# Kernel tuning notes

Measured on AMD Instinct MI355X. Metric: run time of the kernel, lower is better.

## Reference

```python
import jax, jax.numpy as jnp
import numpy as np

N = 400000        # pixel nodes (B images ~224x224)
E = 3200000       # edges, avg degree 8
B = 8             # images
NUM_SP = 150      # superpixels per image (<= 196, per assert)
S = B * NUM_SP    # total superpixel segments
GRID = 14 * 14    # fixed 14x14 grid = 196 slots
DIMS = [24, 8, 16, 32, 64, 64]  # conv_out_dim=24 -> channels//8 ... channels=64


def setup_inputs():
    key = jax.random.key(0)
    ks = jax.random.split(key, 16)
    inp = {}
    inp["x"] = jax.random.normal(ks[0], (N, DIMS[0]), jnp.float32)
    inp["edge_index"] = jax.random.randint(ks[1], (2, E), 0, N, jnp.int32)
    inp["batch_idx"] = jnp.sort(jax.random.randint(ks[2], (N,), 0, S, jnp.int32))
    inp["num_sp"] = jnp.full((B,), NUM_SP, jnp.int32)
    for i in range(5):
        fi, fo = DIMS[i], DIMS[i + 1]
        inp[f"W{i+1}"] = jax.random.normal(ks[3 + i], (fi, fo), jnp.float32) * (2.0 / fi) ** 0.5
        inp[f"b{i+1}"] = jnp.zeros((fo,), jnp.float32)
        inp[f"g{i+1}"] = jnp.ones((fo,), jnp.float32)
        inp[f"be{i+1}"] = jnp.zeros((fo,), jnp.float32)
    C = DIMS[-1]
    inp["Wp"] = jax.random.normal(ks[9], (4 * C, C), jnp.float32) * (2.0 / (4 * C)) ** 0.5
    inp["bp"] = jnp.zeros((C,), jnp.float32)
    return inp


def _forward(x, edge_index, batch_idx, num_sp, layers, Wp, bp):
    n = x.shape[0]
    # GCNConv: add self-loops, symmetric normalization D^-1/2 (A+I) D^-1/2
    loop = jnp.arange(n, dtype=edge_index.dtype)
    src = jnp.concatenate([edge_index[0], loop])
    dst = jnp.concatenate([edge_index[1], loop])
    deg = jax.ops.segment_sum(jnp.ones_like(dst, dtype=jnp.float32), dst, num_segments=n)
    dis = jax.lax.rsqrt(deg)  # deg >= 1 due to self-loops
    norm = dis[src] * dis[dst]  # [E+N]

    h = x
    for i, (W, b, g, be) in enumerate(layers):
        h = h @ W                                                   # [N, fo]
        h = jax.ops.segment_sum(h[src] * norm[:, None], dst, num_segments=n) + b
        # BatchNorm (training mode: batch stats over all nodes)
        mu = h.mean(axis=0)
        var = h.var(axis=0)
        h = g * (h - mu) * jax.lax.rsqrt(var + 1e-5) + be
        if i < 4:  # last BN feeds the aggregator directly (no ReLU)
            h = jax.nn.relu(h)

    # MultiAggregation(['mean','min','max','std'], mode='proj') over superpixel ids
    cnt = jnp.maximum(jax.ops.segment_sum(jnp.ones((n, 1), jnp.float32), batch_idx, num_segments=S), 1.0)
    sm = jax.ops.segment_sum(h, batch_idx, num_segments=S)
    sm2 = jax.ops.segment_sum(h * h, batch_idx, num_segments=S)
    mean = sm / cnt
    std = jnp.sqrt(jax.nn.relu(sm2 / cnt - mean * mean) + 1e-5)  # PyG StdAggregation
    mn = jax.ops.segment_min(h, batch_idx, num_segments=S)
    mx = jax.ops.segment_max(h, batch_idx, num_segments=S)
    agg = jnp.concatenate([mean, mn, mx, std], axis=1) @ Wp + bp  # [S, C]

    # padding_reshape_layer: pack per-image superpixel rows into [B, C, 14, 14]
    offs = jnp.cumsum(num_sp) - num_sp                # start row of each image
    pos = jnp.arange(GRID, dtype=num_sp.dtype)
    idx = jnp.clip(offs[:, None] + pos[None, :], 0, S - 1)  # [B, 196]
    mask = pos[None, :] < num_sp[:, None]
    feats = jnp.where(mask[..., None], agg[idx], 0.0)       # [B, 196, C]
    C = agg.shape[1]
    # torch: reshape(14,14,C) then transpose(0,2) -> y[c,j,i] = x[i,j,c]
    return feats.reshape(B, 14, 14, C).transpose(0, 3, 2, 1)


def reference(x, edge_index, batch_idx, num_sp,
              W1, b1, g1, be1, W2, b2, g2, be2, W3, b3, g3, be3,
              W4, b4, g4, be4, W5, b5, g5, be5, Wp, bp):
    layers = [(W1, b1, g1, be1), (W2, b2, g2, be2), (W3, b3, g3, be3),
              (W4, b4, g4, be4), (W5, b5, g5, be5)]
    return _forward(x, edge_index, batch_idx, num_sp, layers, Wp, bp)
```

## Files before the change

kernel.cpp:

```cpp
#include <hip/hip_runtime.h>
#include <hip/hip_fp16.h>

#define TPB 256
#define BSH 9
#define BUCK (1 << BSH)
#define NBMAX 1024
#define CAP 6144

using f16x8 = __attribute__((ext_vector_type(8))) _Float16;
using f32x4 = __attribute__((ext_vector_type(4))) float;


union H8 { uint4 u; __half2 h[4]; f16x8 f; };
union H4 { uint2 u; __half2 h[2]; };

__device__ inline void h8_to_f(const H8 v, float4& a, float4& b) {
    float2 f0 = __half22float2(v.h[0]);
    float2 f1 = __half22float2(v.h[1]);
    float2 f2 = __half22float2(v.h[2]);
    float2 f3 = __half22float2(v.h[3]);
    a = make_float4(f0.x, f0.y, f1.x, f1.y);
    b = make_float4(f2.x, f2.y, f3.x, f3.y);
}
__device__ inline H8 f_to_h8(float4 a, float4 b) {
    H8 r;
    r.h[0] = __floats2half2_rn(a.x, a.y);
    r.h[1] = __floats2half2_rn(a.z, a.w);
    r.h[2] = __floats2half2_rn(b.x, b.y);
    r.h[3] = __floats2half2_rn(b.z, b.w);
    return r;
}
__device__ inline float4 f4z() { return make_float4(0.f, 0.f, 0.f, 0.f); }
__device__ inline float4 f4axpy(float4 a, float s, float4 c) {
    return make_float4(fmaf(a.x, s, c.x), fmaf(a.y, s, c.y), fmaf(a.z, s, c.z), fmaf(a.w, s, c.w));
}
__device__ inline float4 f4relu_aff(float4 h, float4 sc, float4 sb) {
    return make_float4(fmaxf(fmaf(h.x, sc.x, sb.x), 0.f), fmaxf(fmaf(h.y, sc.y, sb.y), 0.f),
                       fmaxf(fmaf(h.z, sc.z, sb.z), 0.f), fmaxf(fmaf(h.w, sc.w, sb.w), 0.f));
}


__global__ __launch_bounds__(256) void k_bcount(const int* __restrict__ dst, int E,
                                                int* __restrict__ bcount, int nb) {
    __shared__ int hist[NBMAX];
    for (int i = threadIdx.x; i < nb; i += 256) hist[i] = 0;
    __syncthreads();
    const int e0 = blockIdx.x * 8192;
#pragma unroll 4
    for (int k = 0; k < 32; ++k) {
        int e = e0 + k * 256 + threadIdx.x;
        if (e < E) atomicAdd(&hist[dst[e] >> BSH], 1);
    }
    __syncthreads();
    for (int i = threadIdx.x; i < nb; i += 256) {
        int h = hist[i];
        if (h) atomicAdd(&bcount[i], h);
    }
}

__global__ void k_bscan(const int* __restrict__ bcount, int* __restrict__ bbase,
                        int* __restrict__ bcur, int nb, int E, int* __restrict__ row_ptr,
                        int n) {
    if (threadIdx.x == 0 && blockIdx.x == 0) {
        int run = 0;
        for (int i = 0; i < nb; ++i) {
            bbase[i] = run;
            bcur[i] = run;
            run += bcount[i];
        }
        bbase[nb] = E;
        row_ptr[n] = E;
    }
}

__global__ __launch_bounds__(256) void k_partA(const int* __restrict__ src,
                                               const int* __restrict__ dst, int E,
                                               int* __restrict__ bcur, int* __restrict__ bin,
                                               int nb) {
    __shared__ int hist[NBMAX];
    __shared__ int base[NBMAX];
    for (int i = threadIdx.x; i < nb; i += 256) hist[i] = 0;
    __syncthreads();
    const int e0 = blockIdx.x * 8192;
#pragma unroll 4
    for (int k = 0; k < 32; ++k) {
        int e = e0 + k * 256 + threadIdx.x;
        if (e < E) atomicAdd(&hist[dst[e] >> BSH], 1);
    }
    __syncthreads();
    for (int i = threadIdx.x; i < nb; i += 256) {
        int h = hist[i];
        base[i] = h ? atomicAdd(&bcur[i], h) : 0;
        hist[i] = 0;
    }
    __syncthreads();
#pragma unroll 4
    for (int k = 0; k < 32; ++k) {
        int e = e0 + k * 256 + threadIdx.x;
        if (e < E) {
            int d = dst[e];
            int b = d >> BSH;
            int off = atomicAdd(&hist[b], 1);
            bin[base[b] + off] = ((d & (BUCK - 1)) << 19) | src[e];
        }
    }
}

__global__ __launch_bounds__(256) void k_csr_bucket(const int* __restrict__ bin,
                                                    const int* __restrict__ bbase,
                                                    int* __restrict__ row_ptr,
                                                    float* __restrict__ dis,
                                                    int* __restrict__ csr_src, int n) {
    __shared__ int ldeg[BUCK];
    __shared__ int lcur[BUCK];
    __shared__ int ts[256];
    __shared__ int stage[CAP];
    const int b = blockIdx.x;
    const int node0 = b << BSH;
    const int nodes = min(BUCK, n - node0);
    const int ebeg = bbase[b], eend = bbase[b + 1];
    const int cnt = eend - ebeg;

    for (int i = threadIdx.x; i < BUCK; i += 256) ldeg[i] = 0;
    __syncthreads();
    for (int e = ebeg + threadIdx.x; e < eend; e += 256)
        atomicAdd(&ldeg[bin[e] >> 19], 1);
    __syncthreads();

    const int b2 = threadIdx.x * 2;
    int v0 = ldeg[b2], v1 = ldeg[b2 + 1];
    ts[threadIdx.x] = v0 + v1;
    __syncthreads();
    for (int off = 1; off < 256; off <<= 1) {
        int t = (threadIdx.x >= off) ? ts[threadIdx.x - off] : 0;
        __syncthreads();
        ts[threadIdx.x] += t;
        __syncthreads();
    }
    int o0 = (threadIdx.x == 0) ? 0 : ts[threadIdx.x - 1];
    int o1 = o0 + v0;
    lcur[b2] = o0;
    lcur[b2 + 1] = o1;
    if (b2 < nodes) {
        row_ptr[node0 + b2] = ebeg + o0;
        dis[node0 + b2] = rsqrtf((float)(v0 + 1));
    }
    if (b2 + 1 < nodes) {
        row_ptr[node0 + b2 + 1] = ebeg + o1;
        dis[node0 + b2 + 1] = rsqrtf((float)(v1 + 1));
    }
    __syncthreads();

    for (int e = ebeg + threadIdx.x; e < eend; e += 256) {
        int p = bin[e];
        int pos = atomicAdd(&lcur[p >> 19], 1);
        int s = p & 0x7FFFF;
        if (pos < CAP) stage[pos] = s;
        else csr_src[ebeg + pos] = s;
    }
    __syncthreads();
    int m = cnt < CAP ? cnt : CAP;
    for (int i = threadIdx.x; i < m; i += 256) csr_src[ebeg + i] = stage[i];
}


template <int FI, int FO, bool STATS, bool IN_F32>
__global__ __launch_bounds__(TPB) void k_mm_v(const void* __restrict__ tin,
                                              const float* __restrict__ W,
                                              __half* __restrict__ z,
                                              float* __restrict__ stats, int n) {
    constexpr int GROUPS = FO / 8;
    constexpr int NPB = (TPB / GROUPS) * 4;
    __shared__ float sW[FI * FO];
    __shared__ float sred[STATS ? TPB * 16 : 1];
    for (int i = threadIdx.x; i < FI * FO; i += TPB) sW[i] = W[i];
    __syncthreads();

    const int g = threadIdx.x % GROUPS;
    const int nl = threadIdx.x / GROUPS;
    const int nbase = blockIdx.x * NPB + nl * 4;

    float4 acc0[4], acc1[4];
#pragma unroll
    for (int j = 0; j < 4; ++j) { acc0[j] = f4z(); acc1[j] = f4z(); }

    for (int k = 0; k < FI; k += 4) {
        float4 wv0[4], wv1[4];
#pragma unroll
        for (int kk = 0; kk < 4; ++kk) {
            wv0[kk] = *(const float4*)&sW[(k + kk) * FO + g * 8];
            wv1[kk] = *(const float4*)&sW[(k + kk) * FO + g * 8 + 4];
        }
#pragma unroll
        for (int j = 0; j < 4; ++j) {
            int node = nbase + j;
            float rk[4] = {0.f, 0.f, 0.f, 0.f};
            if (node < n) {
                if (IN_F32) {
                    float4 rv = *(const float4*)((const float*)tin + (size_t)node * FI + k);
                    rk[0] = rv.x; rk[1] = rv.y; rk[2] = rv.z; rk[3] = rv.w;
                } else {
                    H4 hv;
                    hv.u = *(const uint2*)((const __half*)tin + (size_t)node * FI + k);
                    float2 f0 = __half22float2(hv.h[0]);
                    float2 f1 = __half22float2(hv.h[1]);
                    rk[0] = f0.x; rk[1] = f0.y; rk[2] = f1.x; rk[3] = f1.y;
                }
            }
#pragma unroll
            for (int kk = 0; kk < 4; ++kk) {
                acc0[j] = f4axpy(wv0[kk], rk[kk], acc0[j]);
                acc1[j] = f4axpy(wv1[kk], rk[kk], acc1[j]);
            }
        }
    }

#pragma unroll
    for (int j = 0; j < 4; ++j) {
        int node = nbase + j;
        if (node < n) {
            H8 o = f_to_h8(acc0[j], acc1[j]);
            *(uint4*)(z + (size_t)node * FO + g * 8) = o.u;
        }
    }

    if (STATS) {
        float4 s0 = f4z(), s1 = f4z(), q0 = f4z(), q1 = f4z();
#pragma unroll
        for (int j = 0; j < 4; ++j) {
            s0.x += acc0[j].x; s0.y += acc0[j].y; s0.z += acc0[j].z; s0.w += acc0[j].w;
            s1.x += acc1[j].x; s1.y += acc1[j].y; s1.z += acc1[j].z; s1.w += acc1[j].w;
            q0.x = fmaf(acc0[j].x, acc0[j].x, q0.x); q0.y = fmaf(acc0[j].y, acc0[j].y, q0.y);
            q0.z = fmaf(acc0[j].z, acc0[j].z, q0.z); q0.w = fmaf(acc0[j].w, acc0[j].w, q0.w);
            q1.x = fmaf(acc1[j].x, acc1[j].x, q1.x); q1.y = fmaf(acc1[j].y, acc1[j].y, q1.y);
            q1.z = fmaf(acc1[j].z, acc1[j].z, q1.z); q1.w = fmaf(acc1[j].w, acc1[j].w, q1.w);
        }
        float* slot = &sred[threadIdx.x * 16];
        *(float4*)(slot + 0) = s0;
        *(float4*)(slot + 4) = s1;
        *(float4*)(slot + 8) = q0;
        *(float4*)(slot + 12) = q1;
        __syncthreads();
        if (threadIdx.x < FO * 2) {
            int c = threadIdx.x % FO;
            int m = threadIdx.x / FO;
            int g2 = c / 8, ci = c % 8;
            float a = 0.f;
            for (int nl2 = 0; nl2 < TPB / GROUPS; ++nl2)
                a += sred[(nl2 * GROUPS + g2) * 16 + m * 8 + ci];
            atomicAdd(&stats[m * FO + c], a);
        }
    }
}


template <int FI, int RT>
__global__ __launch_bounds__(256) void k_gmm(const int* __restrict__ row_ptr,
                                             const int* __restrict__ csr_src,
                                             const float* __restrict__ dis,
                                             const __half* __restrict__ zin,
                                             const float* __restrict__ W,
                                             const float* __restrict__ stats_in,
                                             const float* __restrict__ gg,
                                             const float* __restrict__ be, float inv_n,
                                             __half* __restrict__ zout,
                                             float* __restrict__ stats_out, int n) {
    constexpr int KC = FI / 32;
    constexpr int RSW = FI + 8;
    constexpr int ROWS = 4 * RT * 16;
    __shared__ _Float16 wt[64 * RSW];
    __shared__ float saff[2 * FI];
    __shared__ float sstat[2][4][64];

    for (int i = threadIdx.x; i < FI * 64; i += 256) {
        int k = i >> 6, nn = i & 63;
        wt[nn * RSW + k] = (_Float16)W[i];
    }
    if (threadIdx.x < FI) {
        int c = threadIdx.x;
        float mu = stats_in[c] * inv_n;
        float var = stats_in[FI + c] * inv_n - mu * mu;
        float sv = gg[c] * rsqrtf(var + 1e-5f);
        saff[c] = sv;
        saff[FI + c] = fmaf(-mu, sv, be[c]);
    }
    __syncthreads();

    const int lane = threadIdx.x & 63;
    const int wv = threadIdx.x >> 6;
    const int quad = lane >> 4;
    const int mcol = lane & 15;

    f16x8 bf[4][KC];
#pragma unroll
    for (int t = 0; t < 4; ++t)
#pragma unroll
        for (int c = 0; c < KC; ++c)
            bf[t][c] = *(const f16x8*)&wt[(t * 16 + mcol) * RSW + c * 32 + quad * 8];

    float4 sc[2 * KC], sb[2 * KC];
#pragma unroll
    for (int c = 0; c < KC; ++c) {
        sc[2 * c] = *(const float4*)&saff[c * 32 + quad * 8];
        sc[2 * c + 1] = *(const float4*)&saff[c * 32 + quad * 8 + 4];
        sb[2 * c] = *(const float4*)&saff[FI + c * 32 + quad * 8];
        sb[2 * c + 1] = *(const float4*)&saff[FI + c * 32 + quad * 8 + 4];
    }

    float s[4] = {0.f, 0.f, 0.f, 0.f}, q[4] = {0.f, 0.f, 0.f, 0.f};

#pragma unroll
    for (int rt = 0; rt < RT; ++rt) {
        const int row0 = blockIdx.x * ROWS + wv * (RT * 16) + rt * 16;
        const int node = row0 + mcol;
        float4 acc[2 * KC];
#pragma unroll
        for (int v = 0; v < 2 * KC; ++v) acc[v] = f4z();

        if (node < n) {
            float dn = dis[node];
            float w0 = dn * dn;
#pragma unroll
            for (int c = 0; c < KC; ++c) {
                H8 hv;
                hv.u = *(const uint4*)(zin + (size_t)node * FI + c * 32 + quad * 8);
                float4 a, b;
                h8_to_f(hv, a, b);
                a = f4relu_aff(a, sc[2 * c], sb[2 * c]);
                b = f4relu_aff(b, sc[2 * c + 1], sb[2 * c + 1]);
                acc[2 * c] = f4axpy(a, w0, acc[2 * c]);
                acc[2 * c + 1] = f4axpy(b, w0, acc[2 * c + 1]);
            }
            int beg = row_ptr[node], end = row_ptr[node + 1];
            int j = beg;
            for (; j + 1 < end; j += 2) {
                int s0 = csr_src[j], s1 = csr_src[j + 1];
                float wA = dn * dis[s0];
                float wB = dn * dis[s1];
                uint4 rA[KC], rB[KC];
#pragma unroll
                for (int c = 0; c < KC; ++c) {
                    rA[c] = *(const uint4*)(zin + (size_t)s0 * FI + c * 32 + quad * 8);
                    rB[c] = *(const uint4*)(zin + (size_t)s1 * FI + c * 32 + quad * 8);
                }
#pragma unroll
                for (int c = 0; c < KC; ++c) {
                    H8 hv; float4 a, b;
                    hv.u = rA[c];
                    h8_to_f(hv, a, b);
                    a = f4relu_aff(a, sc[2 * c], sb[2 * c]);
                    b = f4relu_aff(b, sc[2 * c + 1], sb[2 * c + 1]);
                    acc[2 * c] = f4axpy(a, wA, acc[2 * c]);
                    acc[2 * c + 1] = f4axpy(b, wA, acc[2 * c + 1]);
                    hv.u = rB[c];
                    h8_to_f(hv, a, b);
                    a = f4relu_aff(a, sc[2 * c], sb[2 * c]);
                    b = f4relu_aff(b, sc[2 * c + 1], sb[2 * c + 1]);
                    acc[2 * c] = f4axpy(a, wB, acc[2 * c]);
                    acc[2 * c + 1] = f4axpy(b, wB, acc[2 * c + 1]);
                }
            }
            if (j < end) {
                int s0 = csr_src[j];
                float wA = dn * dis[s0];
#pragma unroll
                for (int c = 0; c < KC; ++c) {
                    H8 hv;
                    hv.u = *(const uint4*)(zin + (size_t)s0 * FI + c * 32 + quad * 8);
                    float4 a, b;
                    h8_to_f(hv, a, b);
                    a = f4relu_aff(a, sc[2 * c], sb[2 * c]);
                    b = f4relu_aff(b, sc[2 * c + 1], sb[2 * c + 1]);
                    acc[2 * c] = f4axpy(a, wA, acc[2 * c]);
                    acc[2 * c + 1] = f4axpy(b, wA, acc[2 * c + 1]);
                }
            }
        }

        f16x8 a[KC];
#pragma unroll
        for (int c = 0; c < KC; ++c) {
            H8 cv = f_to_h8(acc[2 * c], acc[2 * c + 1]);
            a[c] = cv.f;
        }
        f32x4 cacc[4];
#pragma unroll
        for (int t = 0; t < 4; ++t) cacc[t] = f32x4{0.f, 0.f, 0.f, 0.f};
#pragma unroll
        for (int t = 0; t < 4; ++t)
#pragma unroll
            for (int c = 0; c < KC; ++c)
                cacc[t] = __builtin_amdgcn_mfma_f32_16x16x32_f16(a[c], bf[t][c], cacc[t], 0, 0, 0);

#pragma unroll
        for (int t = 0; t < 4; ++t)
#pragma unroll
            for (int r = 0; r < 4; ++r) {
                int row = row0 + quad * 4 + r;
                if (row < n) zout[(size_t)row * 64 + t * 16 + mcol] = __float2half(cacc[t][r]);
            }
#pragma unroll
        for (int t = 0; t < 4; ++t) {
            s[t] += cacc[t][0] + cacc[t][1] + cacc[t][2] + cacc[t][3];
            q[t] += cacc[t][0] * cacc[t][0] + cacc[t][1] * cacc[t][1] + cacc[t][2] * cacc[t][2] +
                    cacc[t][3] * cacc[t][3];
        }
    }

#pragma unroll
    for (int off = 16; off < 64; off <<= 1) {
#pragma unroll
        for (int t = 0; t < 4; ++t) {
            s[t] += __shfl_xor(s[t], off, 64);
            q[t] += __shfl_xor(q[t], off, 64);
        }
    }
    if (lane < 16) {
#pragma unroll
        for (int t = 0; t < 4; ++t) {
            sstat[0][wv][t * 16 + lane] = s[t];
            sstat[1][wv][t * 16 + lane] = q[t];
        }
    }
    __syncthreads();
    if (threadIdx.x < 128) {
        int c = threadIdx.x & 63, m = threadIdx.x >> 6;
        float a4 = sstat[m][0][c] + sstat[m][1][c] + sstat[m][2][c] + sstat[m][3][c];
        atomicAdd(&stats_out[m * 64 + c], a4);
    }
}


template <int F, bool AFFINE, bool STATS>
__global__ __launch_bounds__(TPB) void k_gather(const int* __restrict__ row_ptr,
                                                const int* __restrict__ csr_src,
                                                const float* __restrict__ dis,
                                                const __half* __restrict__ z,
                                                __half* __restrict__ t,
                                                const float* __restrict__ stats_in,
                                                const float* __restrict__ gg,
                                                const float* __restrict__ be, float inv_n,
                                                float* __restrict__ stats_out, int n) {
    constexpr int GW = (F < 16) ? F : 16;
    constexpr int PARTS = F / GW;
    constexpr int NV = GW / 4;
    constexpr int NL = GW / 8;
    __shared__ float sred[STATS ? TPB * 16 : 1];
    int tid = blockIdx.x * blockDim.x + threadIdx.x;
    int node = tid / PARTS;
    int part = tid % PARTS;
    bool active = node < n;
    if (!STATS && !active) return;
    const int cbase = part * GW;

    float4 sc[NV], sb[NV];
    if (AFFINE) {
#pragma unroll
        for (int v = 0; v < NV; ++v) {
            float scv[4], sbv[4];
#pragma unroll
            for (int u = 0; u < 4; ++u) {
                int c = cbase + v * 4 + u;
                float mu = stats_in[c] * inv_n;
                float var = stats_in[F + c] * inv_n - mu * mu;
                float s = gg[c] * rsqrtf(var + 1e-5f);
                scv[u] = s;
                sbv[u] = fmaf(-mu, s, be[c]);
            }
            sc[v] = make_float4(scv[0], scv[1], scv[2], scv[3]);
            sb[v] = make_float4(sbv[0], sbv[1], sbv[2], sbv[3]);
        }
    }

    float4 acc[NV];
#pragma unroll
    for (int v = 0; v < NV; ++v) acc[v] = f4z();

    if (active) {
        float dn = dis[node];
        float w0 = dn * dn;
        {
            const uint4* zp = (const uint4*)(z + (size_t)node * F + cbase);
#pragma unroll
            for (int l = 0; l < NL; ++l) {
                H8 hv; hv.u = zp[l];
                float4 a, b;
                h8_to_f(hv, a, b);
                if (AFFINE) { a = f4relu_aff(a, sc[2 * l], sb[2 * l]); b = f4relu_aff(b, sc[2 * l + 1], sb[2 * l + 1]); }
                acc[2 * l] = f4axpy(a, w0, acc[2 * l]);
                acc[2 * l + 1] = f4axpy(b, w0, acc[2 * l + 1]);
            }
        }
        int beg = row_ptr[node], end = row_ptr[node + 1];
        int j = beg;
        for (; j + 3 < end; j += 4) {
            int s0 = csr_src[j], s1 = csr_src[j + 1], s2 = csr_src[j + 2], s3 = csr_src[j + 3];
            float wA = dn * dis[s0];
            float wB = dn * dis[s1];
            float wC = dn * dis[s2];
            float wD = dn * dis[s3];
            const uint4* pA = (const uint4*)(z + (size_t)s0 * F + cbase);
            const uint4* pB = (const uint4*)(z + (size_t)s1 * F + cbase);
            const uint4* pC = (const uint4*)(z + (size_t)s2 * F + cbase);
            const uint4* pD = (const uint4*)(z + (size_t)s3 * F + cbase);
            uint4 rA[NL], rB[NL], rC[NL], rD[NL];
#pragma unroll
            for (int l = 0; l < NL; ++l) { rA[l] = pA[l]; rB[l] = pB[l]; rC[l] = pC[l]; rD[l] = pD[l]; }
#pragma unroll
            for (int l = 0; l < NL; ++l) {
                H8 hv; float4 a, b;
                hv.u = rA[l]; h8_to_f(hv, a, b);
                if (AFFINE) { a = f4relu_aff(a, sc[2 * l], sb[2 * l]); b = f4relu_aff(b, sc[2 * l + 1], sb[2 * l + 1]); }
                acc[2 * l] = f4axpy(a, wA, acc[2 * l]); acc[2 * l + 1] = f4axpy(b, wA, acc[2 * l + 1]);
                hv.u = rB[l]; h8_to_f(hv, a, b);
                if (AFFINE) { a = f4relu_aff(a, sc[2 * l], sb[2 * l]); b = f4relu_aff(b, sc[2 * l + 1], sb[2 * l + 1]); }
                acc[2 * l] = f4axpy(a, wB, acc[2 * l]); acc[2 * l + 1] = f4axpy(b, wB, acc[2 * l + 1]);
                hv.u = rC[l]; h8_to_f(hv, a, b);
                if (AFFINE) { a = f4relu_aff(a, sc[2 * l], sb[2 * l]); b = f4relu_aff(b, sc[2 * l + 1], sb[2 * l + 1]); }
                acc[2 * l] = f4axpy(a, wC, acc[2 * l]); acc[2 * l + 1] = f4axpy(b, wC, acc[2 * l + 1]);
                hv.u = rD[l]; h8_to_f(hv, a, b);
                if (AFFINE) { a = f4relu_aff(a, sc[2 * l], sb[2 * l]); b = f4relu_aff(b, sc[2 * l + 1], sb[2 * l + 1]); }
                acc[2 * l] = f4axpy(a, wD, acc[2 * l]); acc[2 * l + 1] = f4axpy(b, wD, acc[2 * l + 1]);
            }
        }
        for (; j < end; ++j) {
            int s0 = csr_src[j];
            float wA = dn * dis[s0];
            const uint4* pA = (const uint4*)(z + (size_t)s0 * F + cbase);
#pragma unroll
            for (int l = 0; l < NL; ++l) {
                H8 hv; hv.u = pA[l];
                float4 a, b;
                h8_to_f(hv, a, b);
                if (AFFINE) { a = f4relu_aff(a, sc[2 * l], sb[2 * l]); b = f4relu_aff(b, sc[2 * l + 1], sb[2 * l + 1]); }
                acc[2 * l] = f4axpy(a, wA, acc[2 * l]);
                acc[2 * l + 1] = f4axpy(b, wA, acc[2 * l + 1]);
            }
        }
        uint4* tp = (uint4*)(t + (size_t)node * F + cbase);
#pragma unroll
        for (int l = 0; l < NL; ++l) tp[l] = f_to_h8(acc[2 * l], acc[2 * l + 1]).u;
    }

    if (STATS) {
        float* slot = &sred[threadIdx.x * 16];
        *(float4*)(slot + 0) = acc[0];
        *(float4*)(slot + 4) = acc[1];
        float4 q0 = make_float4(acc[0].x * acc[0].x, acc[0].y * acc[0].y, acc[0].z * acc[0].z,
                                acc[0].w * acc[0].w);
        float4 q1 = make_float4(acc[1].x * acc[1].x, acc[1].y * acc[1].y, acc[1].z * acc[1].z,
                                acc[1].w * acc[1].w);
        *(float4*)(slot + 8) = q0;
        *(float4*)(slot + 12) = q1;
        __syncthreads();
        if (threadIdx.x < 16) {
            int c = threadIdx.x % 8;
            int m = threadIdx.x / 8;
            float a = 0.f;
            for (int t2 = 0; t2 < TPB; ++t2) a += sred[t2 * 16 + m * 8 + c];
            atomicAdd(&stats_out[m * 8 + c], a);
        }
    }
}


__device__ inline int bsearch_seg(const int* __restrict__ bidx, int n, int s) {
    int lo = 0, hi = n;
    while (lo < hi) {
        int mid = (lo + hi) >> 1;
        if (bidx[mid] < s) lo = mid + 1; else hi = mid;
    }
    return lo;
}

__global__ __launch_bounds__(TPB) void k_seg_reduce(const __half* __restrict__ z,
                                                    const int* __restrict__ bidx, int n,
                                                    float* __restrict__ aggin,
                                                    const float* __restrict__ stats,
                                                    const float* __restrict__ gg,
                                                    const float* __restrict__ be, float inv_n) {
    __shared__ int sbounds[2];
    int s = blockIdx.x;
    if (threadIdx.x < 2) sbounds[threadIdx.x] = bsearch_seg(bidx, n, s + threadIdx.x);
    __syncthreads();
    int start = sbounds[0], end = sbounds[1];
    int c = threadIdx.x & 63;
    float mu = stats[c] * inv_n;
    float var = stats[64 + c] * inv_n - mu * mu;
    float scv = gg[c] * rsqrtf(var + 1e-5f);
    float sbv = fmaf(-mu, scv, be[c]);
    int r0 = start + (threadIdx.x >> 6);
    float sm = 0.f, sm2 = 0.f, mn = INFINITY, mx = -INFINITY;
    for (int r = r0; r < end; r += 4) {
        float v = fmaf(__half2float(z[(size_t)r * 64 + c]), scv, sbv);
        sm += v;
        sm2 = fmaf(v, v, sm2);
        mn = fminf(mn, v);
        mx = fmaxf(mx, v);
    }
    __shared__ float s_sm[TPB], s_sm2[TPB], s_mn[TPB], s_mx[TPB];
    s_sm[threadIdx.x] = sm;
    s_sm2[threadIdx.x] = sm2;
    s_mn[threadIdx.x] = mn;
    s_mx[threadIdx.x] = mx;
    __syncthreads();
    if (threadIdx.x < 64) {
        for (int t = threadIdx.x + 64; t < TPB; t += 64) {
            sm += s_sm[t];
            sm2 += s_sm2[t];
            mn = fminf(mn, s_mn[t]);
            mx = fmaxf(mx, s_mx[t]);
        }
        int count = end - start;
        float cnt = (float)(count > 0 ? count : 1);
        float mean = sm / cnt;
        float var2 = sm2 / cnt - mean * mean;
        if (var2 < 0.f) var2 = 0.f;
        float sd = sqrtf(var2 + 1e-5f);
        if (count <= 0) { mn = 0.f; mx = 0.f; }
        aggin[s * 256 + c] = mean;
        aggin[s * 256 + 64 + c] = mn;
        aggin[s * 256 + 128 + c] = mx;
        aggin[s * 256 + 192 + c] = sd;
    }
}

__global__ __launch_bounds__(64) void k_proj(const float* __restrict__ aggin,
                                             const float* __restrict__ Wp,
                                             const float* __restrict__ bp,
                                             float* __restrict__ proj) {
    __shared__ float sA[256];
    int s = blockIdx.x;
    int j = threadIdx.x;
    for (int k = j; k < 256; k += 64) sA[k] = aggin[s * 256 + k];
    __syncthreads();
    float acc = bp[j];
#pragma unroll 8
    for (int k = 0; k < 256; ++k) acc = fmaf(sA[k], Wp[k * 64 + j], acc);
    proj[s * 64 + j] = acc;
}

__global__ void k_pack(const float* __restrict__ proj, const int* __restrict__ num_sp,
                       float* __restrict__ out, int B, int S) {
    int idx = blockIdx.x * blockDim.x + threadIdx.x;
    int total = B * 64 * 196;
    if (idx >= total) return;
    int ii = idx % 14;
    int jj = (idx / 14) % 14;
    int c = (idx / 196) % 64;
    int b = idx / (196 * 64);
    int p = ii * 14 + jj;
    int off = 0;
    for (int k = 0; k < b; ++k) off += num_sp[k];
    float v = 0.f;
    if (p < num_sp[b]) {
        int s = off + p;
        if (s > S - 1) s = S - 1;
        v = proj[s * 64 + c];
    }
    out[idx] = v;
}


extern "C" void kernel_launch(void* const* d_in, const int* in_sizes, int n_in,
                              void* d_out, int out_size, void* d_ws, size_t ws_size,
                              hipStream_t stream) {
    const float* x = (const float*)d_in[0];
    const int* ei = (const int*)d_in[1];
    const int* bidx = (const int*)d_in[2];
    const int* num_sp = (const int*)d_in[3];
    const float* Wl[5], * Gl[5], * BEl[5];
    for (int i = 0; i < 5; ++i) {
        Wl[i] = (const float*)d_in[4 + 4 * i];
        Gl[i] = (const float*)d_in[6 + 4 * i];
        BEl[i] = (const float*)d_in[7 + 4 * i];
    }
    const float* Wp = (const float*)d_in[24];
    const float* bp = (const float*)d_in[25];

    const int n = in_sizes[0] / 24;
    const int E = in_sizes[1] / 2;
    const int B = in_sizes[3];
    const int S = 1200;
    const int* src = ei;
    const int* dst = ei + E;
    const float inv_n = 1.0f / (float)n;
    const int nb = (n + BUCK - 1) >> BSH;

    char* w = (char*)d_ws;
    __half* bufZ = (__half*)w;  w += (size_t)n * 64 * 2;
    __half* bufT = (__half*)w;  w += (size_t)n * 64 * 2;
    float* dis = (float*)w;     w += (size_t)n * 4;
    int* row_ptr = (int*)w;     w += (size_t)(n + 64) * 4;
    int* csr_src = (int*)w;     w += (size_t)E * 4;
    int* bin = (int*)w;         w += (size_t)E * 4;
    int* bcount = (int*)w;      w += (size_t)(nb + 64) * 4;
    int* bbase = (int*)w;       w += (size_t)(nb + 64) * 4;
    int* bcur = (int*)w;        w += (size_t)(nb + 64) * 4;
    float* stats_all = (float*)w; w += 5 * 128 * 4;
    float* aggin = (float*)w;   w += (size_t)S * 256 * 4;
    float* proj = (float*)w;    w += (size_t)S * 64 * 4;
    float* st0 = stats_all;
    float* st1 = stats_all + 128;
    float* st2 = stats_all + 256;
    float* st3 = stats_all + 384;
    float* st4 = stats_all + 512;

    hipMemsetAsync(bcount, 0, (size_t)nb * 4, stream);
    hipMemsetAsync(stats_all, 0, 5 * 128 * 4, stream);
    k_bcount<<<(E + 8191) / 8192, 256, 0, stream>>>(dst, E, bcount, nb);
    k_bscan<<<1, 64, 0, stream>>>(bcount, bbase, bcur, nb, E, row_ptr, n);
    k_partA<<<(E + 8191) / 8192, 256, 0, stream>>>(src, dst, E, bcur, bin, nb);
    k_csr_bucket<<<nb, 256, 0, stream>>>(bin, bbase, row_ptr, dis, csr_src, n);

    k_mm_v<24, 8, false, true><<<(n + 1023) / 1024, TPB, 0, stream>>>(x, Wl[0], bufT, nullptr, n);
    k_gather<8, false, true><<<(n + TPB - 1) / TPB, TPB, 0, stream>>>(
        row_ptr, csr_src, dis, bufT, bufZ, nullptr, nullptr, nullptr, inv_n, st0, n);

    k_gather<8, true, false><<<(n + TPB - 1) / TPB, TPB, 0, stream>>>(
        row_ptr, csr_src, dis, bufZ, bufT, st0, Gl[0], BEl[0], inv_n, nullptr, n);
    k_mm_v<8, 16, true, false><<<(n + 511) / 512, TPB, 0, stream>>>(bufT, Wl[1], bufZ, st1, n);

    k_gather<16, true, false><<<(n + TPB - 1) / TPB, TPB, 0, stream>>>(
        row_ptr, csr_src, dis, bufZ, bufT, st1, Gl[1], BEl[1], inv_n, nullptr, n);
    k_mm_v<16, 32, true, false><<<(n + 255) / 256, TPB, 0, stream>>>(bufT, Wl[2], bufZ, st2, n);

    k_gmm<32, 4><<<(n + 255) / 256, 256, 0, stream>>>(
        row_ptr, csr_src, dis, bufZ, Wl[3], st2, Gl[2], BEl[2], inv_n, bufT, st3, n);
    k_gmm<64, 4><<<(n + 255) / 256, 256, 0, stream>>>(
        row_ptr, csr_src, dis, bufT, Wl[4], st3, Gl[3], BEl[3], inv_n, bufZ, st4, n);

    k_seg_reduce<<<S, TPB, 0, stream>>>(bufZ, bidx, n, aggin, st4, Gl[4], BEl[4], inv_n);
    k_proj<<<S, 64, 0, stream>>>(aggin, Wp, bp, proj);
    int total_out = B * 64 * 196;
    k_pack<<<(total_out + TPB - 1) / TPB, TPB, 0, stream>>>(proj, num_sp, (float*)d_out, B, S);
}
```

Baseline: 967.7 us.

## Split gather columns across lanes and stage aggregated rows through LDS for MFMA

The fused gather+GEMM kernel now splits feature columns across the four 16-lane groups, so each lane gathers only a quarter of each neighbor row. Previously each lane gathered its own quad's slice across all K chunks. The partial rows are written to a per-wave LDS tile and reloaded in MFMA A-fragment layout. B fragments are now read from LDS inside the MFMA loop instead of being held in registers. Rows per block are halved, which doubles the grid. The goal is lower register pressure, higher occupancy and more memory parallelism in the irregular gather, at the cost of extra LDS traffic and a wave-local LDS handoff that relies only on an lgkmcnt wait.

```diff
diff --git a/kernel.cpp b/kernel.cpp
--- a/kernel.cpp
+++ b/kernel.cpp
@@ -267,8 +267,13 @@
                                              float* __restrict__ stats_out, int n) {
     constexpr int KC = FI / 32;
     constexpr int RSW = FI + 8;
+    constexpr int CW = FI / 4;
+    constexpr int NV = CW / 4;
+    constexpr int LPE = CW / 8;
+    constexpr int UN = (LPE == 1) ? 4 : 2;
     constexpr int ROWS = 4 * RT * 16;
     __shared__ _Float16 wt[64 * RSW];
+    __shared__ _Float16 tt[4][16 * RSW];
     __shared__ float saff[2 * FI];
     __shared__ float sstat[2][4][64];
 
@@ -290,107 +295,107 @@
     const int wv = threadIdx.x >> 6;
     const int quad = lane >> 4;
     const int mcol = lane & 15;
-
-    f16x8 bf[4][KC];
-#pragma unroll
-    for (int t = 0; t < 4; ++t)
-#pragma unroll
-        for (int c = 0; c < KC; ++c)
-            bf[t][c] = *(const f16x8*)&wt[(t * 16 + mcol) * RSW + c * 32 + quad * 8];
-
-    float4 sc[2 * KC], sb[2 * KC];
-#pragma unroll
-    for (int c = 0; c < KC; ++c) {
-        sc[2 * c] = *(const float4*)&saff[c * 32 + quad * 8];
-        sc[2 * c + 1] = *(const float4*)&saff[c * 32 + quad * 8 + 4];
-        sb[2 * c] = *(const float4*)&saff[FI + c * 32 + quad * 8];
-        sb[2 * c + 1] = *(const float4*)&saff[FI + c * 32 + quad * 8 + 4];
-    }
+    const int m = lane & 15;
+    const int part = lane >> 4;
+    const int cbase = part * CW;
 
     float s[4] = {0.f, 0.f, 0.f, 0.f}, q[4] = {0.f, 0.f, 0.f, 0.f};
 
-#pragma unroll
     for (int rt = 0; rt < RT; ++rt) {
         const int row0 = blockIdx.x * ROWS + wv * (RT * 16) + rt * 16;
-        const int node = row0 + mcol;
-        float4 acc[2 * KC];
-#pragma unroll
-        for (int v = 0; v < 2 * KC; ++v) acc[v] = f4z();
-
-        if (node < n) {
-            float dn = dis[node];
-            float w0 = dn * dn;
-#pragma unroll
-            for (int c = 0; c < KC; ++c) {
-                H8 hv;
-                hv.u = *(const uint4*)(zin + (size_t)node * FI + c * 32 + quad * 8);
-                float4 a, b;
-                h8_to_f(hv, a, b);
-                a = f4relu_aff(a, sc[2 * c], sb[2 * c]);
-                b = f4relu_aff(b, sc[2 * c + 1], sb[2 * c + 1]);
-                acc[2 * c] = f4axpy(a, w0, acc[2 * c]);
-                acc[2 * c + 1] = f4axpy(b, w0, acc[2 * c + 1]);
-            }
-            int beg = row_ptr[node], end = row_ptr[node + 1];
-            int j = beg;
-            for (; j + 1 < end; j += 2) {
-                int s0 = csr_src[j], s1 = csr_src[j + 1];
-                float wA = dn * dis[s0];
-                float wB = dn * dis[s1];
-                uint4 rA[KC], rB[KC];
-#pragma unroll
-                for (int c = 0; c < KC; ++c) {
-                    rA[c] = *(const uint4*)(zin + (size_t)s0 * FI + c * 32 + quad * 8);
-                    rB[c] = *(const uint4*)(zin + (size_t)s1 * FI + c * 32 + quad * 8);
-                }
-#pragma unroll
-                for (int c = 0; c < KC; ++c) {
-                    H8 hv; float4 a, b;
-                    hv.u = rA[c];
-                    h8_to_f(hv, a, b);
-                    a = f4relu_aff(a, sc[2 * c], sb[2 * c]);
-                    b = f4relu_aff(b, sc[2 * c + 1], sb[2 * c + 1]);
-                    acc[2 * c] = f4axpy(a, wA, acc[2 * c]);
-                    acc[2 * c + 1] = f4axpy(b, wA, acc[2 * c + 1]);
-                    hv.u = rB[c];
-                    h8_to_f(hv, a, b);
-                    a = f4relu_aff(a, sc[2 * c], sb[2 * c]);
-                    b = f4relu_aff(b, sc[2 * c + 1], sb[2 * c + 1]);
-                    acc[2 * c] = f4axpy(a, wB, acc[2 * c]);
-                    acc[2 * c + 1] = f4axpy(b, wB, acc[2 * c + 1]);
-                }
-            }
-            if (j < end) {
-                int s0 = csr_src[j];
-                float wA = dn * dis[s0];
-#pragma unroll
-                for (int c = 0; c < KC; ++c) {
+
+        float4 acc[NV];
+#pragma unroll
+        for (int v = 0; v < NV; ++v) acc[v] = f4z();
+        {
+            float4 sc[NV], sb[NV];
+#pragma unroll
+            for (int v = 0; v < NV; ++v) {
+                sc[v] = *(const float4*)&saff[cbase + v * 4];
+                sb[v] = *(const float4*)&saff[FI + cbase + v * 4];
+            }
+            const int node = row0 + m;
+            if (node < n) {
+                float dn = dis[node];
+                float w0 = dn * dn;
+#pragma unroll
+                for (int l = 0; l < LPE; ++l) {
                     H8 hv;
-                    hv.u = *(const uint4*)(zin + (size_t)s0 * FI + c * 32 + quad * 8);
+                    hv.u = *(const uint4*)(zin + (size_t)node * FI + cbase + l * 8);
                     float4 a, b;
                     h8_to_f(hv, a, b);
-                    a = f4relu_aff(a, sc[2 * c], sb[2 * c]);
-                    b = f4relu_aff(b, sc[2 * c + 1], sb[2 * c + 1]);
-                    acc[2 * c] = f4axpy(a, wA, acc[2 * c]);
-                    acc[2 * c + 1] = f4axpy(b, wA, acc[2 * c + 1]);
+                    a = f4relu_aff(a, sc[2 * l], sb[2 * l]);
+                    b = f4relu_aff(b, sc[2 * l + 1], sb[2 * l + 1]);
+                    acc[2 * l] = f4axpy(a, w0, acc[2 * l]);
+                    acc[2 * l + 1] = f4axpy(b, w0, acc[2 * l + 1]);
                 }
-            }
-        }
+                int beg = row_ptr[node], end = row_ptr[node + 1];
+                int j = beg;
+                for (; j + UN - 1 < end; j += UN) {
+                    int sidx[UN];
+                    float wgt[UN];
+                    uint4 r[UN][LPE];
+#pragma unroll
+                    for (int u = 0; u < UN; ++u) sidx[u] = csr_src[j + u];
+#pragma unroll
+                    for (int u = 0; u < UN; ++u) wgt[u] = dn * dis[sidx[u]];
+#pragma unroll
+                    for (int u = 0; u < UN; ++u)
+#pragma unroll
+                        for (int l = 0; l < LPE; ++l)
+                            r[u][l] = *(const uint4*)(zin + (size_t)sidx[u] * FI + cbase + l * 8);
+#pragma unroll
+                    for (int u = 0; u < UN; ++u)
+#pragma unroll
+                        for (int l = 0; l < LPE; ++l) {
+                            H8 hv; hv.u = r[u][l];
+                            float4 a, b;
+                            h8_to_f(hv, a, b);
+                            a = f4relu_aff(a, sc[2 * l], sb[2 * l]);
+                            b = f4relu_aff(b, sc[2 * l + 1], sb[2 * l + 1]);
+                            acc[2 * l] = f4axpy(a, wgt[u], acc[2 * l]);
+                            acc[2 * l + 1] = f4axpy(b, wgt[u], acc[2 * l + 1]);
+                        }
+                }
+                for (; j < end; ++j) {
+                    int s0 = csr_src[j];
+                    float wA = dn * dis[s0];
+#pragma unroll
+                    for (int l = 0; l < LPE; ++l) {
+                        H8 hv;
+                        hv.u = *(const uint4*)(zin + (size_t)s0 * FI + cbase + l * 8);
+                        float4 a, b;
+                        h8_to_f(hv, a, b);
+                        a = f4relu_aff(a, sc[2 * l], sb[2 * l]);
+                        b = f4relu_aff(b, sc[2 * l + 1], sb[2 * l + 1]);
+                        acc[2 * l] = f4axpy(a, wA, acc[2 * l]);
+                        acc[2 * l + 1] = f4axpy(b, wA, acc[2 * l + 1]);
+                    }
+                }
+            }
+        }
+        {
+            _Float16* tp = &tt[wv][m * RSW + cbase];
+#pragma unroll
+            for (int l = 0; l < LPE; ++l)
+                *(uint4*)(tp + l * 8) = f_to_h8(acc[2 * l], acc[2 * l + 1]).u;
+        }
+        asm volatile("s_waitcnt lgkmcnt(0)" ::: "memory");
 
         f16x8 a[KC];
 #pragma unroll
-        for (int c = 0; c < KC; ++c) {
-            H8 cv = f_to_h8(acc[2 * c], acc[2 * c + 1]);
-            a[c] = cv.f;
-        }
+        for (int c = 0; c < KC; ++c)
+            a[c] = *(const f16x8*)&tt[wv][mcol * RSW + c * 32 + quad * 8];
         f32x4 cacc[4];
 #pragma unroll
         for (int t = 0; t < 4; ++t) cacc[t] = f32x4{0.f, 0.f, 0.f, 0.f};
 #pragma unroll
         for (int t = 0; t < 4; ++t)
 #pragma unroll
-            for (int c = 0; c < KC; ++c)
-                cacc[t] = __builtin_amdgcn_mfma_f32_16x16x32_f16(a[c], bf[t][c], cacc[t], 0, 0, 0);
+            for (int c = 0; c < KC; ++c) {
+                f16x8 bfv = *(const f16x8*)&wt[(t * 16 + mcol) * RSW + c * 32 + quad * 8];
+                cacc[t] = __builtin_amdgcn_mfma_f32_16x16x32_f16(a[c], bfv, cacc[t], 0, 0, 0);
+            }
 
 #pragma unroll
         for (int t = 0; t < 4; ++t)
@@ -424,9 +429,9 @@
     }
     __syncthreads();
     if (threadIdx.x < 128) {
-        int c = threadIdx.x & 63, m = threadIdx.x >> 6;
-        float a4 = sstat[m][0][c] + sstat[m][1][c] + sstat[m][2][c] + sstat[m][3][c];
-        atomicAdd(&stats_out[m * 64 + c], a4);
+        int c = threadIdx.x & 63, mm = threadIdx.x >> 6;
+        float a4 = sstat[mm][0][c] + sstat[mm][1][c] + sstat[mm][2][c] + sstat[mm][3][c];
+        atomicAdd(&stats_out[mm * 64 + c], a4);
     }
 }
 
@@ -725,9 +730,9 @@
         row_ptr, csr_src, dis, bufZ, bufT, st1, Gl[1], BEl[1], inv_n, nullptr, n);
     k_mm_v<16, 32, true, false><<<(n + 255) / 256, TPB, 0, stream>>>(bufT, Wl[2], bufZ, st2, n);
 
-    k_gmm<32, 4><<<(n + 255) / 256, 256, 0, stream>>>(
+    k_gmm<32, 2><<<(n + 127) / 128, 256, 0, stream>>>(
         row_ptr, csr_src, dis, bufZ, Wl[3], st2, Gl[2], BEl[2], inv_n, bufT, st3, n);
-    k_gmm<64, 4><<<(n + 255) / 256, 256, 0, stream>>>(
+    k_gmm<64, 2><<<(n + 127) / 128, 256, 0, stream>>>(
         row_ptr, csr_src, dis, bufT, Wl[4], st3, Gl[3], BEl[3], inv_n, bufZ, st4, n);
 
     k_seg_reduce<<<S, TPB, 0, stream>>>(bufZ, bidx, n, aggin, st4, Gl[4], BEl[4], inv_n);
```

After: 976.8 us. About the same (+0.9%).
